# Kernel tuning notes

Measured on AMD Instinct MI355X. Metric: run time of the kernel, lower is better.

The kernel has to match this reference:

```python
import jax, jax.numpy as jnp
import numpy as np

B, C, T, H, W = 4, 256, 8, 28, 28
IC = 128  # inter_channels = in_channels // 2


def setup_inputs() -> dict:
    key = jax.random.key(0)
    ks = jax.random.split(key, 5)
    s_in = 1.0 / np.sqrt(C)
    s_ic = 1.0 / np.sqrt(IC)
    return {
        "x": jax.random.normal(ks[0], (B, C, T, H, W), dtype=jnp.float32),
        "Wg": jax.random.normal(ks[1], (IC, C), dtype=jnp.float32) * s_in,
        "Wtheta": jax.random.normal(ks[2], (IC, C), dtype=jnp.float32) * s_in,
        "Wphi": jax.random.normal(ks[3], (IC, C), dtype=jnp.float32) * s_in,
        "Wz": jax.random.normal(ks[4], (C, IC), dtype=jnp.float32) * s_ic,
    }


def reference(x, Wg, Wtheta, Wphi, Wz):
    b, c, t, h, w = x.shape
    n = t * h * w
    xf = x.reshape(b, c, n)  # 1x1x1 conv == channel GEMM over flattened positions
    g_x = jnp.einsum("oc,bcn->bon", Wg, xf)       # [B, IC, N]
    theta_x = jnp.einsum("oc,bcn->bon", Wtheta, xf)
    phi_x = jnp.einsum("oc,bcn->bon", Wphi, xf)
    # f = theta^T @ phi : [B, N, N]
    f = jnp.einsum("bcn,bcm->bnm", theta_x, phi_x)
    f_div_C = jax.nn.softmax(f, axis=-1)
    # y = f_div_C @ g^T : [B, N, IC] -> keep as [B, IC, N]
    y = jnp.einsum("bnm,bcm->bcn", f_div_C, g_x)  # [B, IC, N]
    z = jnp.einsum("oc,bcn->bon", Wz, y).reshape(b, c, t, h, w) + x
    return z
```

## Files before the change

### kernel.cpp

```cpp
#include <hip/hip_runtime.h>
#include <cstdint>


#define BB   4
#define CCH  256
#define NPOS 6272
#define ICH  128
#define BNIC ((size_t)BB * NPOS * ICH)
#define TKF  32
#define SLACK 12.0f

typedef __attribute__((ext_vector_type(8)))  _Float16 h8v;
typedef __attribute__((ext_vector_type(16))) float fx16;

__device__ __forceinline__ unsigned short f2h(float f) {
  _Float16 h = (_Float16)f;
  return __builtin_bit_cast(unsigned short, h);
}
__device__ __forceinline__ unsigned int pkh(float lo, float hi) {
  return __builtin_bit_cast(unsigned int, __builtin_amdgcn_cvt_pkrtz(lo, hi));
}
__device__ __forceinline__ float h2f(unsigned short u) {
  return (float)__builtin_bit_cast(_Float16, u);
}

__global__ __launch_bounds__(256, 1)
void wconv(const float* __restrict__ Wtheta, const float* __restrict__ Wphi,
           const float* __restrict__ Wg,
           unsigned short* __restrict__ Whi, unsigned short* __restrict__ Wlo) {
  const int idx4 = (blockIdx.x * 256 + threadIdx.x) * 4;
  const int p = idx4 >> 15;
  const float* W = (p == 0) ? Wtheta : (p == 1) ? Wphi : Wg;
  const float4 v = *(const float4*)&W[idx4 - (p << 15)];
  const float vv[4] = {v.x, v.y, v.z, v.w};
  ushort4 h, l;
  unsigned short* hp = (unsigned short*)&h;
  unsigned short* lp = (unsigned short*)&l;
  #pragma unroll
  for (int q = 0; q < 4; ++q) {
    _Float16 hh = (_Float16)vv[q];
    hp[q] = __builtin_bit_cast(unsigned short, hh);
    lp[q] = f2h(vv[q] - (float)hh);
  }
  *(ushort4*)&Whi[idx4] = h;
  *(ushort4*)&Wlo[idx4] = l;
}

__global__ __launch_bounds__(256, 2)
void proj_mfma(const float* __restrict__ x,
               const unsigned short* __restrict__ Whi,
               const unsigned short* __restrict__ Wlo,
               unsigned short* __restrict__ Qg,
               unsigned short* __restrict__ Kg,
               unsigned short* __restrict__ Vtg) {
  __shared__ unsigned short Xhi[32][40];
  __shared__ unsigned short Xlo[32][40];
  const int n0 = blockIdx.x * 32;
  const int b  = blockIdx.y;
  const int tid = threadIdx.x;
  const int lane = tid & 63, wv = tid >> 6;
  const int ln = lane & 31, g = lane >> 5;

  fx16 acc[3];
  acc[0] = (fx16)(0.0f); acc[1] = (fx16)(0.0f); acc[2] = (fx16)(0.0f);

  const int sn = tid & 31, cq = (tid >> 5) * 4;
  const float* xp = x + ((size_t)b * CCH + cq) * NPOS + n0 + sn;

  float pv[4];
  #pragma unroll
  for (int q = 0; q < 4; ++q) pv[q] = xp[(size_t)q * NPOS];

  for (int c0 = 0; c0 < CCH; c0 += 32) {
    {
      ushort4 h4, l4;
      unsigned short* hp = (unsigned short*)&h4;
      unsigned short* lp = (unsigned short*)&l4;
      #pragma unroll
      for (int q = 0; q < 4; ++q) {
        _Float16 hh = (_Float16)pv[q];
        hp[q] = __builtin_bit_cast(unsigned short, hh);
        lp[q] = f2h(pv[q] - (float)hh);
      }
      *(ushort4*)&Xhi[sn][cq] = h4;
      *(ushort4*)&Xlo[sn][cq] = l4;
    }
    if (c0 + 32 < CCH) {
      #pragma unroll
      for (int q = 0; q < 4; ++q) pv[q] = xp[(size_t)(c0 + 32 + q) * NPOS];
    }
    __syncthreads();
    #pragma unroll
    for (int kc = 0; kc < 2; ++kc) {
      const h8v bxh = *(const h8v*)&Xhi[ln][kc * 16 + g * 8];
      const h8v bxl = *(const h8v*)&Xlo[ln][kc * 16 + g * 8];
      #pragma unroll
      for (int t = 0; t < 3; ++t) {
        const int T = wv * 3 + t;
        const size_t wb = ((size_t)(T * 32 + ln)) * CCH + c0 + kc * 16 + g * 8;
        const h8v ah = *(const h8v*)&Whi[wb];
        const h8v al = *(const h8v*)&Wlo[wb];
        acc[t] = __builtin_amdgcn_mfma_f32_32x32x16_f16(ah, bxh, acc[t], 0, 0, 0);
        acc[t] = __builtin_amdgcn_mfma_f32_32x32x16_f16(ah, bxl, acc[t], 0, 0, 0);
        acc[t] = __builtin_amdgcn_mfma_f32_32x32x16_f16(al, bxh, acc[t], 0, 0, 0);
      }
    }
    __syncthreads();
  }

  const float LOG2E = 1.4426950408889634f;
  const int n = n0 + ln;
  #pragma unroll
  for (int t = 0; t < 3; ++t) {
    const int T = wv * 3 + t;
    const int p = T >> 2;
    const int ot = (T & 3) * 32;
    if (p < 2) {
      unsigned short* Out = (p == 0) ? Qg : Kg;
      const float scl = (p == 0) ? LOG2E : 1.0f;
      #pragma unroll
      for (int q = 0; q < 4; ++q) {
        ushort4 v;
        v.x = f2h(acc[t][4 * q + 0] * scl);
        v.y = f2h(acc[t][4 * q + 1] * scl);
        v.z = f2h(acc[t][4 * q + 2] * scl);
        v.w = f2h(acc[t][4 * q + 3] * scl);
        *(ushort4*)&Out[((size_t)b * NPOS + n) * ICH + ot + 8 * q + 4 * g] = v;
      }
    } else {
      #pragma unroll
      for (int r = 0; r < 16; ++r) {
        const int o = ot + (r & 3) + 8 * (r >> 2) + 4 * g;
        Vtg[((size_t)b * ICH + o) * NPOS + n] = f2h(acc[t][r]);
      }
    }
  }
}

template <int KS>
__global__ __launch_bounds__(256, 2)
void flash_t(const unsigned short* __restrict__ Qg,
             const unsigned short* __restrict__ Kg,
             const unsigned short* __restrict__ Vtg,
             unsigned short* __restrict__ Opart,
             float* __restrict__ Mpart,
             float* __restrict__ Lpart) {
  constexpr int KLEN = NPOS / KS;
  constexpr int NIT  = KLEN / TKF;
  __shared__ unsigned short Ks[2][TKF * 128];
  __shared__ unsigned short Vs[2][128 * 36];

  const int b   = blockIdx.z;
  const int spl = blockIdx.y;
  const int n0  = blockIdx.x * 128;
  const int kb  = spl * KLEN;
  const int tid = threadIdx.x;
  const int lane = tid & 63, wv = tid >> 6;
  const int qlane = lane & 31, g = lane >> 5;
  const int swz = qlane & 15;

  h8v qf[8];
  {
    const size_t qbase = ((size_t)b * NPOS + n0 + 32 * wv + qlane) * ICH;
    #pragma unroll
    for (int cs = 0; cs < 8; ++cs)
      qf[cs] = *(const h8v*)&Qg[qbase + cs * 16 + g * 8];
  }

  {
    #pragma unroll
    for (int i = 0; i < 2; ++i) {
      const int kr = (tid >> 4) + i * 16, c = tid & 15;
      const uint4 v = *(const uint4*)&Kg[((size_t)b * NPOS + kb + kr) * ICH + c * 8];
      *(uint4*)&Ks[0][kr * 128 + (c ^ (kr & 15)) * 8] = v;
      const int idx = tid * 2 + i, dr = idx >> 2, cv = idx & 3;
      const uint4 w = *(const uint4*)&Vtg[((size_t)b * ICH + dr) * NPOS + kb + cv * 8];
      *(uint2*)&Vs[0][dr * 36 + cv * 8]     = make_uint2(w.x, w.y);
      *(uint2*)&Vs[0][dr * 36 + cv * 8 + 4] = make_uint2(w.z, w.w);
    }
  }
  __syncthreads();

  float m_run = -1e30f, m_true = -1e30f, l_run = 0.0f;
  fx16 accO[4];
  #pragma unroll
  for (int mt = 0; mt < 4; ++mt) accO[mt] = (fx16)(0.0f);

  uint4 stgK[2], stgV[2];

  for (int it = 0; it < NIT; ++it) {
    const int cur = it & 1;
    const bool pre = (it + 1 < NIT);
    if (pre) {
      const int k0n = kb + (it + 1) * TKF;
      #pragma unroll
      for (int i = 0; i < 2; ++i) {
        const int kr = (tid >> 4) + i * 16;
        stgK[i] = *(const uint4*)&Kg[((size_t)b * NPOS + k0n + kr) * ICH + (tid & 15) * 8];
        const int idx = tid * 2 + i, dr = idx >> 2, cv = idx & 3;
        stgV[i] = *(const uint4*)&Vtg[((size_t)b * ICH + dr) * NPOS + k0n + cv * 8];
      }
    }

    fx16 accS = (fx16)(0.0f);
    #pragma unroll
    for (int cs = 0; cs < 8; ++cs) {
      const h8v aK = *(const h8v*)&Ks[cur][qlane * 128 + ((2 * cs + g) ^ swz) * 8];
      accS = __builtin_amdgcn_mfma_f32_32x32x16_f16(aK, qf[cs], accS, 0, 0, 0);
    }

    float a0 = fmaxf(accS[0], accS[1]),   a1 = fmaxf(accS[2], accS[3]);
    float a2 = fmaxf(accS[4], accS[5]),   a3 = fmaxf(accS[6], accS[7]);
    float a4 = fmaxf(accS[8], accS[9]),   a5 = fmaxf(accS[10], accS[11]);
    float a6 = fmaxf(accS[12], accS[13]), a7 = fmaxf(accS[14], accS[15]);
    a0 = fmaxf(a0, a1); a2 = fmaxf(a2, a3); a4 = fmaxf(a4, a5); a6 = fmaxf(a6, a7);
    float mx = fmaxf(fmaxf(a0, a2), fmaxf(a4, a6));
    mx = fmaxf(mx, __shfl_xor(mx, 32));
    m_true = fmaxf(m_true, mx);
    const bool fold = __any(mx > m_run + SLACK);
    const float mn = fold ? fmaxf(m_run, mx) : m_run;
    float lsum = 0.0f;
    unsigned int pk[4][2];
    #pragma unroll
    for (int u = 0; u < 4; ++u) {
      const float p0 = exp2f(accS[4 * u + 0] - mn);
      const float p1 = exp2f(accS[4 * u + 1] - mn);
      const float p2 = exp2f(accS[4 * u + 2] - mn);
      const float p3 = exp2f(accS[4 * u + 3] - mn);
      lsum += (p0 + p1) + (p2 + p3);
      pk[u][0] = pkh(p0, p1);
      pk[u][1] = pkh(p2, p3);
    }
    lsum += __shfl_xor(lsum, 32);
    if (fold) {
      const float alpha = exp2f(m_run - mn);
      l_run = l_run * alpha + lsum;
      m_run = mn;
      #pragma unroll
      for (int mt = 0; mt < 4; ++mt)
        #pragma unroll
        for (int r = 0; r < 16; ++r) accO[mt][r] *= alpha;
    } else {
      l_run += lsum;
    }

    #pragma unroll
    for (int s = 0; s < 2; ++s) {
      const unsigned int s0 = pk[2 * s + (g ^ 1)][0];
      const unsigned int s1 = pk[2 * s + (g ^ 1)][1];
      const unsigned int t0 = __shfl_xor(s0, 32);
      const unsigned int t1 = __shfl_xor(s1, 32);
      union { unsigned int u[4]; h8v v; } bP;
      bP.u[0] = g ? t0 : pk[2 * s][0];
      bP.u[1] = g ? t1 : pk[2 * s][1];
      bP.u[2] = g ? pk[2 * s + 1][0] : t0;
      bP.u[3] = g ? pk[2 * s + 1][1] : t1;
      #pragma unroll
      for (int mt = 0; mt < 4; ++mt) {
        const int dr = 32 * mt + qlane;
        union { unsigned int u[4]; h8v v; } aV;
        const uint2 lo = *(const uint2*)&Vs[cur][dr * 36 + (2 * s + g) * 8];
        const uint2 hi = *(const uint2*)&Vs[cur][dr * 36 + (2 * s + g) * 8 + 4];
        aV.u[0] = lo.x; aV.u[1] = lo.y; aV.u[2] = hi.x; aV.u[3] = hi.y;
        accO[mt] = __builtin_amdgcn_mfma_f32_32x32x16_f16(aV.v, bP.v, accO[mt], 0, 0, 0);
      }
    }

    if (pre) {
      const int nb = cur ^ 1;
      #pragma unroll
      for (int i = 0; i < 2; ++i) {
        const int kr = (tid >> 4) + i * 16;
        *(uint4*)&Ks[nb][kr * 128 + ((tid & 15) ^ (kr & 15)) * 8] = stgK[i];
        const int idx = tid * 2 + i, dr = idx >> 2, cv = idx & 3;
        *(uint2*)&Vs[nb][dr * 36 + cv * 8]     = make_uint2(stgV[i].x, stgV[i].y);
        *(uint2*)&Vs[nb][dr * 36 + cv * 8 + 4] = make_uint2(stgV[i].z, stgV[i].w);
      }
    }
    __syncthreads();
  }

  const float scale = exp2f(m_run - m_true);
  const int ncol = n0 + 32 * wv + qlane;
  const size_t obase = (size_t)(b * KS + spl) * ICH * NPOS;
  #pragma unroll
  for (int mt = 0; mt < 4; ++mt)
    #pragma unroll
    for (int r = 0; r < 16; ++r) {
      const int d = 32 * mt + (r & 3) + 8 * (r >> 2) + 4 * g;
      Opart[obase + (size_t)d * NPOS + ncol] = f2h(accO[mt][r] * scale);
    }
  if (g == 0) {
    Mpart[(size_t)(b * KS + spl) * NPOS + ncol] = m_true;
    Lpart[(size_t)(b * KS + spl) * NPOS + ncol] = l_run * scale;
  }
}

template <int KS>
__global__ __launch_bounds__(256, 2)
void mz_t(const float* __restrict__ x,
          const float* __restrict__ Wz,
          const unsigned short* __restrict__ Opart,
          const float* __restrict__ Mpart,
          const float* __restrict__ Lpart,
          float* __restrict__ out) {
  __shared__ float wgt[128][8];
  __shared__ unsigned short Yh[128][24], Yl[128][24];
  __shared__ unsigned short Wzh[128][24], Wzl[128][24];

  const int n0 = blockIdx.x * 128;
  const int c0 = blockIdx.y * 128;
  const int b  = blockIdx.z;
  const int tid = threadIdx.x;
  const int lane = tid & 63, wv = tid >> 6;
  const int ln = lane & 31, g = lane >> 5;

  if (tid < 128) {
    const int n = n0 + tid;
    float m[KS], l[KS];
    float M0 = -1e30f;
    #pragma unroll
    for (int s = 0; s < KS; ++s) {
      m[s] = Mpart[(size_t)(b * KS + s) * NPOS + n];
      l[s] = Lpart[(size_t)(b * KS + s) * NPOS + n];
      M0 = fmaxf(M0, m[s]);
    }
    float w[KS], lt = 0.0f;
    #pragma unroll
    for (int s = 0; s < KS; ++s) { w[s] = exp2f(m[s] - M0); lt += w[s] * l[s]; }
    const float inv = 1.0f / lt;
    #pragma unroll
    for (int s = 0; s < KS; ++s) wgt[tid][s] = w[s] * inv;
  }
  __syncthreads();

  const int np  = tid & 63;
  const int icg = tid >> 6;
  float wA[KS], wB[KS];
  #pragma unroll
  for (int s = 0; s < KS; ++s) { wA[s] = wgt[2 * np][s]; wB[s] = wgt[2 * np + 1][s]; }
  const int wc = tid >> 1, wh = (tid & 1) * 8;
  const float* Wzrow = Wz + (size_t)(c0 + wc) * ICH + wh;
  const int cpair = wv >> 1, npair = wv & 1;

  fx16 acc[2][2];
  acc[0][0] = (fx16)(0.0f); acc[0][1] = (fx16)(0.0f);
  acc[1][0] = (fx16)(0.0f); acc[1][1] = (fx16)(0.0f);

  for (int k0 = 0; k0 < ICH; k0 += 16) {
    {
      const float4 w0 = *(const float4*)&Wzrow[k0];
      const float4 w1 = *(const float4*)&Wzrow[k0 + 4];
      const float wv8[8] = {w0.x, w0.y, w0.z, w0.w, w1.x, w1.y, w1.z, w1.w};
      unsigned int hu[4], lu[4];
      #pragma unroll
      for (int q = 0; q < 4; ++q) {
        _Float16 h0 = (_Float16)wv8[2 * q], h1 = (_Float16)wv8[2 * q + 1];
        hu[q] = (unsigned int)__builtin_bit_cast(unsigned short, h0) |
                ((unsigned int)__builtin_bit_cast(unsigned short, h1) << 16);
        lu[q] = (unsigned int)f2h(wv8[2 * q] - (float)h0) |
                ((unsigned int)f2h(wv8[2 * q + 1] - (float)h1) << 16);
      }
      *(uint4*)&Wzh[wc][wh] = make_uint4(hu[0], hu[1], hu[2], hu[3]);
      *(uint4*)&Wzl[wc][wh] = make_uint4(lu[0], lu[1], lu[2], lu[3]);
    }
    {
      unsigned short h0a[4], h1a[4], l0a[4], l1a[4];
      #pragma unroll
      for (int j = 0; j < 4; ++j) {
        const int ic = k0 + icg * 4 + j;
        float y0 = 0.0f, y1 = 0.0f;
        #pragma unroll
        for (int s = 0; s < KS; ++s) {
          const unsigned int u = *(const unsigned int*)
            &Opart[((size_t)(b * KS + s) * ICH + ic) * NPOS + n0 + 2 * np];
          y0 += wA[s] * h2f((unsigned short)(u & 0xffff));
          y1 += wB[s] * h2f((unsigned short)(u >> 16));
        }
        _Float16 hh0 = (_Float16)y0, hh1 = (_Float16)y1;
        h0a[j] = __builtin_bit_cast(unsigned short, hh0);
        h1a[j] = __builtin_bit_cast(unsigned short, hh1);
        l0a[j] = f2h(y0 - (float)hh0);
        l1a[j] = f2h(y1 - (float)hh1);
      }
      const int kc = icg * 4;
      *(uint2*)&Yh[2 * np][kc] = make_uint2(
        (unsigned)h0a[0] | ((unsigned)h0a[1] << 16),
        (unsigned)h0a[2] | ((unsigned)h0a[3] << 16));
      *(uint2*)&Yh[2 * np + 1][kc] = make_uint2(
        (unsigned)h1a[0] | ((unsigned)h1a[1] << 16),
        (unsigned)h1a[2] | ((unsigned)h1a[3] << 16));
      *(uint2*)&Yl[2 * np][kc] = make_uint2(
        (unsigned)l0a[0] | ((unsigned)l0a[1] << 16),
        (unsigned)l0a[2] | ((unsigned)l0a[3] << 16));
      *(uint2*)&Yl[2 * np + 1][kc] = make_uint2(
        (unsigned)l1a[0] | ((unsigned)l1a[1] << 16),
        (unsigned)l1a[2] | ((unsigned)l1a[3] << 16));
    }
    __syncthreads();

    h8v Ah[2], Al[2], Bh[2], Bl[2];
    #pragma unroll
    for (int ci = 0; ci < 2; ++ci) {
      const int cr = (cpair * 2 + ci) * 32 + ln;
      Ah[ci] = *(const h8v*)&Wzh[cr][g * 8];
      Al[ci] = *(const h8v*)&Wzl[cr][g * 8];
    }
    #pragma unroll
    for (int ni = 0; ni < 2; ++ni) {
      const int nr = (npair * 2 + ni) * 32 + ln;
      Bh[ni] = *(const h8v*)&Yh[nr][g * 8];
      Bl[ni] = *(const h8v*)&Yl[nr][g * 8];
    }
    #pragma unroll
    for (int ci = 0; ci < 2; ++ci)
      #pragma unroll
      for (int ni = 0; ni < 2; ++ni) {
        acc[ci][ni] = __builtin_amdgcn_mfma_f32_32x32x16_f16(Ah[ci], Bh[ni], acc[ci][ni], 0, 0, 0);
        acc[ci][ni] = __builtin_amdgcn_mfma_f32_32x32x16_f16(Ah[ci], Bl[ni], acc[ci][ni], 0, 0, 0);
        acc[ci][ni] = __builtin_amdgcn_mfma_f32_32x32x16_f16(Al[ci], Bh[ni], acc[ci][ni], 0, 0, 0);
      }
    __syncthreads();
  }

  #pragma unroll
  for (int ci = 0; ci < 2; ++ci)
    #pragma unroll
    for (int ni = 0; ni < 2; ++ni) {
      const int n = n0 + npair * 64 + ni * 32 + ln;
      #pragma unroll
      for (int r = 0; r < 16; ++r) {
        const int c = c0 + cpair * 64 + ci * 32 + (r & 3) + 8 * (r >> 2) + 4 * g;
        const size_t base = ((size_t)(b * CCH + c)) * NPOS + n;
        out[base] = acc[ci][ni][r] + x[base];
      }
    }
}

extern "C" void kernel_launch(void* const* d_in, const int* in_sizes, int n_in,
                              void* d_out, int out_size, void* d_ws, size_t ws_size,
                              hipStream_t stream) {
  const float* x      = (const float*)d_in[0];
  const float* Wg     = (const float*)d_in[1];
  const float* Wtheta = (const float*)d_in[2];
  const float* Wphi   = (const float*)d_in[3];
  const float* Wz     = (const float*)d_in[4];
  float* out = (float*)d_out;

  unsigned short* Qg    = (unsigned short*)d_ws;
  unsigned short* Kg    = Qg + BNIC;
  unsigned short* Vtg   = Kg + BNIC;
  unsigned short* Opart = Vtg + BNIC;

  unsigned short* Whi = Opart;
  unsigned short* Wlo = Whi + 3 * 128 * 256;

  wconv<<<dim3(96), 256, 0, stream>>>(Wtheta, Wphi, Wg, Whi, Wlo);
  proj_mfma<<<dim3(NPOS / 32, BB), 256, 0, stream>>>(x, Whi, Wlo, Qg, Kg, Vtg);

  const size_t need7 = (3 + 7) * BNIC * 2 + (size_t)2 * 7 * BB * NPOS * 4;
  if (ws_size >= need7) {
    constexpr int KS = 7;
    float* Mpart = (float*)(Opart + (size_t)KS * BNIC);
    float* Lpart = Mpart + (size_t)KS * BB * NPOS;
    flash_t<KS><<<dim3(NPOS / 128, KS, BB), 256, 0, stream>>>(Qg, Kg, Vtg, Opart, Mpart, Lpart);
    mz_t<KS><<<dim3(NPOS / 128, CCH / 128, BB), 256, 0, stream>>>(x, Wz, Opart, Mpart, Lpart, out);
  } else {
    constexpr int KS = 4;
    float* Mpart = (float*)(Opart + (size_t)KS * BNIC);
    float* Lpart = Mpart + (size_t)KS * BB * NPOS;
    flash_t<KS><<<dim3(NPOS / 128, KS, BB), 256, 0, stream>>>(Qg, Kg, Vtg, Opart, Mpart, Lpart);
    mz_t<KS><<<dim3(NPOS / 128, CCH / 128, BB), 256, 0, stream>>>(x, Wz, Opart, Mpart, Lpart, out);
  }
}
```

Baseline: 311.0 us.

## Halve mz tile width to 64 positions and raise flash occupancy hint

The merge+Wz projection kernel now processes 64 positions per block instead of 128, with each wave owning one 32-channel row of MFMA tiles. This doubles the grid and cuts per-block accumulators and shared memory, aiming for more parallelism and occupancy. In exchange each Wz tile is converted and loaded twice as often. The flash kernel's launch bounds go from 2 to 3 waves per SIMD, which may force register spills.

```diff
diff --git a/kernel.cpp b/kernel.cpp
--- a/kernel.cpp
+++ b/kernel.cpp
@@ -138,7 +138,7 @@
 }
 
 template <int KS>
-__global__ __launch_bounds__(256, 2)
+__global__ __launch_bounds__(256, 3)
 void flash_t(const unsigned short* __restrict__ Qg,
              const unsigned short* __restrict__ Kg,
              const unsigned short* __restrict__ Vtg,
@@ -304,18 +304,18 @@
           const float* __restrict__ Mpart,
           const float* __restrict__ Lpart,
           float* __restrict__ out) {
-  __shared__ float wgt[128][8];
-  __shared__ unsigned short Yh[128][24], Yl[128][24];
+  __shared__ float wgt[64][8];
+  __shared__ unsigned short Yh[64][24], Yl[64][24];
   __shared__ unsigned short Wzh[128][24], Wzl[128][24];
 
-  const int n0 = blockIdx.x * 128;
+  const int n0 = blockIdx.x * 64;
   const int c0 = blockIdx.y * 128;
   const int b  = blockIdx.z;
   const int tid = threadIdx.x;
   const int lane = tid & 63, wv = tid >> 6;
   const int ln = lane & 31, g = lane >> 5;
 
-  if (tid < 128) {
+  if (tid < 64) {
     const int n = n0 + tid;
     float m[KS], l[KS];
     float M0 = -1e30f;
@@ -334,18 +334,16 @@
   }
   __syncthreads();
 
-  const int np  = tid & 63;
-  const int icg = tid >> 6;
+  const int np  = tid & 31;
+  const int icg = tid >> 5;
   float wA[KS], wB[KS];
   #pragma unroll
   for (int s = 0; s < KS; ++s) { wA[s] = wgt[2 * np][s]; wB[s] = wgt[2 * np + 1][s]; }
   const int wc = tid >> 1, wh = (tid & 1) * 8;
   const float* Wzrow = Wz + (size_t)(c0 + wc) * ICH + wh;
-  const int cpair = wv >> 1, npair = wv & 1;
-
-  fx16 acc[2][2];
-  acc[0][0] = (fx16)(0.0f); acc[0][1] = (fx16)(0.0f);
-  acc[1][0] = (fx16)(0.0f); acc[1][1] = (fx16)(0.0f);
+
+  fx16 acc[2];
+  acc[0] = (fx16)(0.0f); acc[1] = (fx16)(0.0f);
 
   for (int k0 = 0; k0 < ICH; k0 += 16) {
     {
@@ -365,10 +363,10 @@
       *(uint4*)&Wzl[wc][wh] = make_uint4(lu[0], lu[1], lu[2], lu[3]);
     }
     {
-      unsigned short h0a[4], h1a[4], l0a[4], l1a[4];
-      #pragma unroll
-      for (int j = 0; j < 4; ++j) {
-        const int ic = k0 + icg * 4 + j;
+      unsigned short h0a[2], h1a[2], l0a[2], l1a[2];
+      #pragma unroll
+      for (int j = 0; j < 2; ++j) {
+        const int ic = k0 + icg * 2 + j;
         float y0 = 0.0f, y1 = 0.0f;
         #pragma unroll
         for (int s = 0; s < KS; ++s) {
@@ -383,58 +381,39 @@
         l0a[j] = f2h(y0 - (float)hh0);
         l1a[j] = f2h(y1 - (float)hh1);
       }
-      const int kc = icg * 4;
-      *(uint2*)&Yh[2 * np][kc] = make_uint2(
-        (unsigned)h0a[0] | ((unsigned)h0a[1] << 16),
-        (unsigned)h0a[2] | ((unsigned)h0a[3] << 16));
-      *(uint2*)&Yh[2 * np + 1][kc] = make_uint2(
-        (unsigned)h1a[0] | ((unsigned)h1a[1] << 16),
-        (unsigned)h1a[2] | ((unsigned)h1a[3] << 16));
-      *(uint2*)&Yl[2 * np][kc] = make_uint2(
-        (unsigned)l0a[0] | ((unsigned)l0a[1] << 16),
-        (unsigned)l0a[2] | ((unsigned)l0a[3] << 16));
-      *(uint2*)&Yl[2 * np + 1][kc] = make_uint2(
-        (unsigned)l1a[0] | ((unsigned)l1a[1] << 16),
-        (unsigned)l1a[2] | ((unsigned)l1a[3] << 16));
+      const int kc = icg * 2;
+      *(ushort2*)&Yh[2 * np][kc]     = make_ushort2(h0a[0], h0a[1]);
+      *(ushort2*)&Yh[2 * np + 1][kc] = make_ushort2(h1a[0], h1a[1]);
+      *(ushort2*)&Yl[2 * np][kc]     = make_ushort2(l0a[0], l0a[1]);
+      *(ushort2*)&Yl[2 * np + 1][kc] = make_ushort2(l1a[0], l1a[1]);
     }
     __syncthreads();
 
-    h8v Ah[2], Al[2], Bh[2], Bl[2];
-    #pragma unroll
-    for (int ci = 0; ci < 2; ++ci) {
-      const int cr = (cpair * 2 + ci) * 32 + ln;
-      Ah[ci] = *(const h8v*)&Wzh[cr][g * 8];
-      Al[ci] = *(const h8v*)&Wzl[cr][g * 8];
-    }
+    const int cr = wv * 32 + ln;
+    const h8v Ah = *(const h8v*)&Wzh[cr][g * 8];
+    const h8v Al = *(const h8v*)&Wzl[cr][g * 8];
     #pragma unroll
     for (int ni = 0; ni < 2; ++ni) {
-      const int nr = (npair * 2 + ni) * 32 + ln;
-      Bh[ni] = *(const h8v*)&Yh[nr][g * 8];
-      Bl[ni] = *(const h8v*)&Yl[nr][g * 8];
-    }
-    #pragma unroll
-    for (int ci = 0; ci < 2; ++ci)
-      #pragma unroll
-      for (int ni = 0; ni < 2; ++ni) {
-        acc[ci][ni] = __builtin_amdgcn_mfma_f32_32x32x16_f16(Ah[ci], Bh[ni], acc[ci][ni], 0, 0, 0);
-        acc[ci][ni] = __builtin_amdgcn_mfma_f32_32x32x16_f16(Ah[ci], Bl[ni], acc[ci][ni], 0, 0, 0);
-        acc[ci][ni] = __builtin_amdgcn_mfma_f32_32x32x16_f16(Al[ci], Bh[ni], acc[ci][ni], 0, 0, 0);
-      }
+      const int nr = ni * 32 + ln;
+      const h8v Bh = *(const h8v*)&Yh[nr][g * 8];
+      const h8v Bl = *(const h8v*)&Yl[nr][g * 8];
+      acc[ni] = __builtin_amdgcn_mfma_f32_32x32x16_f16(Ah, Bh, acc[ni], 0, 0, 0);
+      acc[ni] = __builtin_amdgcn_mfma_f32_32x32x16_f16(Ah, Bl, acc[ni], 0, 0, 0);
+      acc[ni] = __builtin_amdgcn_mfma_f32_32x32x16_f16(Al, Bh, acc[ni], 0, 0, 0);
+    }
     __syncthreads();
   }
 
   #pragma unroll
-  for (int ci = 0; ci < 2; ++ci)
-    #pragma unroll
-    for (int ni = 0; ni < 2; ++ni) {
-      const int n = n0 + npair * 64 + ni * 32 + ln;
-      #pragma unroll
-      for (int r = 0; r < 16; ++r) {
-        const int c = c0 + cpair * 64 + ci * 32 + (r & 3) + 8 * (r >> 2) + 4 * g;
-        const size_t base = ((size_t)(b * CCH + c)) * NPOS + n;
-        out[base] = acc[ci][ni][r] + x[base];
-      }
-    }
+  for (int ni = 0; ni < 2; ++ni) {
+    const int n = n0 + ni * 32 + ln;
+    #pragma unroll
+    for (int r = 0; r < 16; ++r) {
+      const int c = c0 + wv * 32 + (r & 3) + 8 * (r >> 2) + 4 * g;
+      const size_t base = ((size_t)(b * CCH + c)) * NPOS + n;
+      out[base] = acc[ni][r] + x[base];
+    }
+  }
 }
 
 extern "C" void kernel_launch(void* const* d_in, const int* in_sizes, int n_in,
@@ -464,12 +443,12 @@
     float* Mpart = (float*)(Opart + (size_t)KS * BNIC);
     float* Lpart = Mpart + (size_t)KS * BB * NPOS;
     flash_t<KS><<<dim3(NPOS / 128, KS, BB), 256, 0, stream>>>(Qg, Kg, Vtg, Opart, Mpart, Lpart);
-    mz_t<KS><<<dim3(NPOS / 128, CCH / 128, BB), 256, 0, stream>>>(x, Wz, Opart, Mpart, Lpart, out);
+    mz_t<KS><<<dim3(NPOS / 64, CCH / 128, BB), 256, 0, stream>>>(x, Wz, Opart, Mpart, Lpart, out);
   } else {
     constexpr int KS = 4;
     float* Mpart = (float*)(Opart + (size_t)KS * BNIC);
     float* Lpart = Mpart + (size_t)KS * BB * NPOS;
     flash_t<KS><<<dim3(NPOS / 128, KS, BB), 256, 0, stream>>>(Qg, Kg, Vtg, Opart, Mpart, Lpart);
-    mz_t<KS><<<dim3(NPOS / 128, CCH / 128, BB), 256, 0, stream>>>(x, Wz, Opart, Mpart, Lpart, out);
-  }
-}
+    mz_t<KS><<<dim3(NPOS / 64, CCH / 128, BB), 256, 0, stream>>>(x, Wz, Opart, Mpart, Lpart, out);
+  }
+}
```

Result: faster. 295.8 us (-4.9%).
